# Kernel optimization log

Hardware: AMD Instinct MI355X
Metric: run time of the kernel (lower is better)

## Reference

```python
import jax, jax.numpy as jnp
import numpy as np

M_RANGE = 3
K = 2 * M_RANGE + 1          # kernel size = 7
N_CLASS = K * K              # 49 motion classes
IM_CHANNEL = 3


def setup_inputs() -> dict:
    key = jax.random.key(0)
    k1, k2, k3, k4 = jax.random.split(key, 4)
    B, H, W = 16, 256, 256
    im_input = jax.random.normal(k1, (B, 2 * IM_CHANNEL, H, W), dtype=jnp.float32)
    im_output = jax.random.normal(k2, (B, IM_CHANNEL, H, W), dtype=jnp.float32)
    # motion in [-M_RANGE, M_RANGE-1) so that floor(m)+M_RANGE+1 <= K-1 (valid bin)
    gt_motion = jax.random.uniform(k3, (B, 2, H, W), dtype=jnp.float32) * (2 * M_RANGE - 1) - M_RANGE
    # grouped-conv weight (already in post-swapaxes [n_class, 1, K, K] layout)
    m_kernel = jax.random.uniform(k4, (N_CLASS, 1, K, K), dtype=jnp.float32)
    return {"im_input": im_input, "im_output": im_output,
            "gt_motion": gt_motion, "m_kernel": m_kernel}


def _axis_weights(m):
    # m: [B,H,W] -> bilinear binning weights over K bins: [B,H,W,K]
    f = jnp.floor(m)
    frac = m - f
    idx = f.astype(jnp.int32) + M_RANGE
    oh0 = jax.nn.one_hot(idx, K, dtype=m.dtype)
    oh1 = jax.nn.one_hot(idx + 1, K, dtype=m.dtype)
    return (1.0 - frac)[..., None] * oh0 + frac[..., None] * oh1


def motion2mask(motion):
    # faithful vectorization of the triple-loop: mask[c=iy*K+ix] = b[iy]*a[ix]
    ax = _axis_weights(motion[:, 0])   # x-motion -> columns of ger(b, a)
    ay = _axis_weights(motion[:, 1])   # y-motion -> rows
    mask = ay[..., :, None] * ax[..., None, :]       # [B,H,W,K,K] outer product
    B, H, W = motion.shape[0], motion.shape[2], motion.shape[3]
    return mask.reshape(B, H, W, N_CLASS).transpose(0, 3, 1, 2)  # [B,N_CLASS,H,W]


def _conv(x, w, groups):
    return jax.lax.conv_general_dilated(
        x, w, window_strides=(1, 1),
        padding=[(M_RANGE, M_RANGE), (M_RANGE, M_RANGE)],
        dimension_numbers=("NCHW", "OIHW", "NCHW"),
        feature_group_count=groups)


def reference(im_input, im_output, gt_motion, m_kernel):
    m_mask = motion2mask(gt_motion)                   # [B,N_CLASS,H,W]
    out_mask = _conv(m_mask, m_kernel, N_CLASS)       # grouped conv, same shape
    im = im_input[:, -IM_CHANNEL:]                    # [B,3,H,W]
    B, C, H, W = im.shape
    # construct_image: each channel expanded to N_CLASS copies then grouped-conv
    # == plain conv of each single channel with all N_CLASS kernels
    nearby = _conv(im.reshape(B * C, 1, H, W), m_kernel, 1)
    nearby = nearby.reshape(B, C, N_CLASS, H, W)
    pred = (nearby * out_mask[:, None]).sum(axis=2)   # [B,3,H,W]
    return pred, m_mask
```

## Files before the change

### kernel.cpp

```cpp
#include <hip/hip_runtime.h>
#include <hip/hip_fp16.h>

typedef _Float16 f16x8 __attribute__((ext_vector_type(8)));
typedef float    f32x4 __attribute__((ext_vector_type(4)));

#define TILE   16
#define HALO   22
#define KK     7
#define NCLASS 49
#define IMW    256
#define IMH    256
#define HW     65536
#define HH     484
#define NV     42
#define WHST   52

#define OFF_OMV    0
#define OFF_HALOF  10752
#define OFF_HALOB  11236
#define OFF_KV     11357
#define SH_TOTAL   13415
#define OFF_IML64  10752
#define OFF_IML32  11720

__device__ __forceinline__ unsigned h2u(__half2 h) { union { __half2 h; unsigned u; } c; c.h = h; return c.u; }
__device__ __forceinline__ __half2  u2h(unsigned u) { union { __half2 h; unsigned u; } c; c.u = u; return c.h; }

__global__ __launch_bounds__(256, 3)
void gtnet_kernel(const float* __restrict__ im_input,
                  const float* __restrict__ gt_motion,
                  const float* __restrict__ m_kernel,
                  float* __restrict__ out_pred,
                  float* __restrict__ out_mask)
{
    __shared__ __align__(16) unsigned SH[SH_TOTAL];
    unsigned*      const omV    = SH + OFF_OMV;
    unsigned*      const haloF  = SH + OFF_HALOF;
    unsigned char* const haloB8 = (unsigned char*)(SH + OFF_HALOB);
    unsigned*      const KV     = SH + OFF_KV;
    float2*        const iml64  = (float2*)(SH + OFF_IML64);
    float*         const iml32  = (float*)(SH + OFF_IML32);
    __half*        const Whf    = (__half*)SH;

    const int tid  = threadIdx.x;
    const int lane = tid & 63, wv_id = tid >> 6;
    const int tx = tid & 15, ty = tid >> 4;
    const int x0 = blockIdx.x * TILE, y0 = blockIdx.y * TILE;
    const int b  = blockIdx.z;
    const int x = x0 + tx, y = y0 + ty;

    const float* mot_x = gt_motion + (size_t)b * 2 * HW;
    const float* mot_y = mot_x + HW;
    const float* imP   = im_input + ((size_t)b * 6 + 3) * HW;

    float2 imr01[2]; float imr2[2];
    #pragma unroll
    for (int k = 0; k < 2; k++) {
        int i = tid + k * 256;
        float2 v01 = make_float2(0.0f, 0.0f); float v2 = 0.0f;
        if (i < HH) {
            int hy = i / HALO, hx = i - hy * HALO;
            int gy = y0 - 3 + hy, gx = x0 - 3 + hx;
            if (gy >= 0 && gy < IMH && gx >= 0 && gx < IMW) {
                int off = gy * IMW + gx;
                v01.x = imP[off];
                v01.y = imP[off + HW];
                v2    = imP[off + 2 * HW];
            }
        }
        imr01[k] = v01; imr2[k] = v2;
    }

    for (int i = tid; i < NCLASS * NV; i += 256) {
        int s = i / NV, n = i - s * NV;
        float k0 = m_kernel[n * NCLASS + s];
        float k7 = m_kernel[(n + KK) * NCLASS + s];
        KV[i] = h2u(__halves2half2(__float2half_rn(k0), __float2half_rn(k7)));
    }
    #pragma unroll
    for (int k = 0; k < 2; k++) {
        int i = tid + k * 256;
        if (i < HH) {
            int hy = i / HALO, hx = i - hy * HALO;
            int gy = y0 - 3 + hy, gx = x0 - 3 + hx;
            unsigned pf = 0u, n4b = 255u;
            if (gy >= 0 && gy < IMH && gx >= 0 && gx < IMW) {
                int off = gy * IMW + gx;
                float ay = mot_y[off] + 3.0f;
                float ax = mot_x[off] + 3.0f;
                float iyf = floorf(ay), ixf = floorf(ax);
                float fy = ay - iyf,    fx = ax - ixf;
                int n00 = (int)iyf * KK + (int)ixf;
                n00 = (n00 < 0) ? 0 : ((n00 > 40) ? 40 : n00);
                pf  = h2u(__halves2half2(__float2half_rn(fy), __float2half_rn(fx)));
                n4b = (unsigned)(n00 * 4);
            }
            haloF[i]  = pf;
            haloB8[i] = (unsigned char)n4b;
        }
    }
    {
        uint4* p = reinterpret_cast<uint4*>(omV);
        for (int i = tid; i < (2 * NV * 128) / 4; i += 256) p[i] = make_uint4(0, 0, 0, 0);
    }

    __syncthreads();

    {
        int off = y * IMW + x;
        float ay = mot_y[off] + 3.0f;
        float ax = mot_x[off] + 3.0f;
        float iyf = floorf(ay), ixf = floorf(ax);
        float fy = ay - iyf,    fx = ax - ixf;
        int   iy = (int)iyf,    ix = (int)ixf;
        float wyA[KK], wxB[KK];
        #pragma unroll
        for (int a = 0; a < KK; a++) {
            wyA[a] = (a == iy) ? (1.0f - fy) : ((a == iy + 1) ? fy : 0.0f);
            wxB[a] = (a == ix) ? (1.0f - fx) : ((a == ix + 1) ? fx : 0.0f);
        }
        float* mm = out_mask + (size_t)b * NCLASS * HW + off;
        #pragma unroll
        for (int a = 0; a < KK; a++)
            #pragma unroll
            for (int bb = 0; bb < KK; bb++)
                mm[(size_t)(a * KK + bb) * HW] = wyA[a] * wxB[bb];
    }

    unsigned* const omHalf = omV + (tid >> 7) * (NV * 128) + (tid & 127);
    const __half hone = __float2half_rn(1.0f);
    #pragma unroll
    for (int u = 0; u < KK; u++) {
        #pragma unroll
        for (int v = 0; v < KK; v++) {
            const int s = u * KK + v;
            const int q = (ty + u) * HALO + (tx + v);
            unsigned pf  = haloF[q];
            unsigned n4u = (unsigned)haloB8[q];
            unsigned n4  = (n4u == 255u) ? 0u : n4u;
            __half2 f2 = u2h(pf);
            __half fy = __low2half(f2), fx = __high2half(f2);
            unsigned wyb = h2u(__halves2half2(__hsub(hone, fy), fy));
            wyb = (n4u == 255u) ? 0u : wyb;
            __half2 wy  = u2h(wyb);
            __half2 wxl = __half2half2(__hsub(hone, fx));
            __half2 wxh = __half2half2(fx);
            const unsigned* kp =
                (const unsigned*)((const char*)KV + s * (NV * 4) + n4);
            unsigned kvA = kp[0], kvB = kp[1];
            unsigned* ob = (unsigned*)((char*)omHalf + n4 * 128);
            unsigned o0 = ob[0], o1 = ob[128];
            __half2 cA = __hmul2(__hmul2(wy, wxl), u2h(kvA));
            __half2 cB = __hmul2(__hmul2(wy, wxh), u2h(kvB));
            ob[0]   = h2u(__hadd2(u2h(o0), cA));
            ob[128] = h2u(__hadd2(u2h(o1), cB));
        }
    }

    __syncthreads();

    #pragma unroll
    for (int k = 0; k < 2; k++) {
        int i = tid + k * 256;
        if (i < HH) { iml64[i] = imr01[k]; iml32[i] = imr2[k]; }
    }

    f16x8 bfr[2][4];
    #pragma unroll
    for (int kit = 0; kit < 2; kit++) {
        #pragma unroll
        for (int nt = 0; nt < 4; nt++) {
            int t  = nt * 16 + (lane & 15);
            int tc = (t > 48) ? 48 : t;
            int k0 = kit * 32 + (lane >> 4) * 8;
            union { unsigned u[4]; f16x8 v; } bu;
            #pragma unroll
            for (int j = 0; j < 4; j++) {
                int c0 = k0 + 2 * j;
                float lo = (c0 <= 48) ? m_kernel[c0 * NCLASS + tc]       : 0.0f;
                float hi = (c0 <= 47) ? m_kernel[(c0 + 1) * NCLASS + tc] : 0.0f;
                bu.u[j] = h2u(__halves2half2(__float2half_rn(lo), __float2half_rn(hi)));
            }
            bfr[kit][nt] = bu.v;
        }
    }

    f16x8 af[2][4];
    #pragma unroll
    for (int kit = 0; kit < 2; kit++) {
        #pragma unroll
        for (int mt = 0; mt < 4; mt++) {
            int k0  = kit * 32 + (lane >> 4) * 8;
            int px  = wv_id * 64 + mt * 16 + (lane & 15);
            const unsigned* pxb = omV + (px >> 7) * (NV * 128) + (px & 127);
            union { unsigned u[4]; f16x8 v; } au;
            #pragma unroll
            for (int j = 0; j < 4; j++) {
                int c0 = k0 + 2 * j;
                int rl = (c0 > 40) ? 40 : c0;
                unsigned d0 = pxb[rl * 128], d1 = pxb[rl * 128 + 128];
                unsigned loM = (d0 & 0xffffu) | (d1 << 16);
                loM = (c0 <= 40) ? loM : 0u;
                int r0 = c0 - 7; r0 = (r0 < 0) ? 0 : ((r0 > 41) ? 41 : r0);
                int r1 = c0 - 6; r1 = (r1 < 0) ? 0 : ((r1 > 41) ? 41 : r1);
                unsigned e0 = pxb[r0 * 128];
                unsigned e1 = pxb[r1 * 128];
                e0 = (c0 >= 8 && c0 <= 48) ? e0 : 0u;
                e1 = (c0 >= 6 && c0 <= 48) ? e1 : 0u;
                unsigned hiM = (e0 >> 16) | (e1 & 0xffff0000u);
                au.u[j] = h2u(__hadd2(u2h(loM), u2h(hiM)));
            }
            af[kit][mt] = au.v;
        }
    }

    __syncthreads();

    f32x4 acc[4][4];
    #pragma unroll
    for (int mt = 0; mt < 4; mt++) {
        #pragma unroll
        for (int nt = 0; nt < 4; nt++) {
            f32x4 c = {0.0f, 0.0f, 0.0f, 0.0f};
            c = __builtin_amdgcn_mfma_f32_16x16x32_f16(af[0][mt], bfr[0][nt], c, 0, 0, 0);
            c = __builtin_amdgcn_mfma_f32_16x16x32_f16(af[1][mt], bfr[1][nt], c, 0, 0, 0);
            acc[mt][nt] = c;
        }
    }

    #pragma unroll
    for (int mt = 0; mt < 4; mt++) {
        #pragma unroll
        for (int nt = 0; nt < 4; nt++) {
            int t = nt * 16 + (lane & 15);
            if (t < NCLASS) {
                #pragma unroll
                for (int r = 0; r < 4; r++) {
                    int px = wv_id * 64 + mt * 16 + (lane >> 4) * 4 + r;
                    Whf[px * WHST + t] = __float2half_rn(acc[mt][nt][r]);
                }
            }
        }
    }

    __syncthreads();

    union { uint2 v[13]; __half h[52]; } wr;
    const uint2* wp = (const uint2*)(Whf + tid * WHST);
    #pragma unroll
    for (int c = 0; c < 13; c++) wr.v[c] = wp[c];

    float a0 = 0.0f, a1 = 0.0f, a2 = 0.0f;
    #pragma unroll
    for (int p = 0; p < KK; p++) {
        #pragma unroll
        for (int qq = 0; qq < KK; qq++) {
            float wvv = __half2float(wr.h[p * KK + qq]);
            int   hq  = (ty + p) * HALO + (tx + qq);
            float2 i01 = iml64[hq];
            float  i2  = iml32[hq];
            a0 = fmaf(wvv, i01.x, a0);
            a1 = fmaf(wvv, i01.y, a1);
            a2 = fmaf(wvv, i2,    a2);
        }
    }
    float* pr = out_pred + (size_t)b * 3 * HW + y * IMW + x;
    pr[0]      = a0;
    pr[HW]     = a1;
    pr[2 * HW] = a2;
}

extern "C" void kernel_launch(void* const* d_in, const int* in_sizes, int n_in,
                              void* d_out, int out_size, void* d_ws, size_t ws_size,
                              hipStream_t stream) {
    const float* im_input  = (const float*)d_in[0];
    const float* gt_motion = (const float*)d_in[2];
    const float* m_kernel  = (const float*)d_in[3];

    float* pred = (float*)d_out;
    float* mask = pred + (size_t)16 * 3 * HW;

    dim3 grid(IMW / TILE, IMH / TILE, 16);
    dim3 block(256);
    hipLaunchKernelGGL(gtnet_kernel, grid, block, 0, stream,
                       im_input, gt_motion, m_kernel, pred, mask);
}
```

Baseline: 343.7 us.

## Restructure MFMA K-dimension to use packed mask words directly and pack weight stores

Result: faster. 336.7 us (-2.1%).

```diff
diff --git a/kernel.cpp b/kernel.cpp
--- a/kernel.cpp
+++ b/kernel.cpp
@@ -13,7 +13,7 @@
 #define HW     65536
 #define HH     484
 #define NV     42
-#define WHST   52
+#define WROW   34
 
 #define OFF_OMV    0
 #define OFF_HALOF  10752
@@ -40,7 +40,6 @@
     unsigned*      const KV     = SH + OFF_KV;
     float2*        const iml64  = (float2*)(SH + OFF_IML64);
     float*         const iml32  = (float*)(SH + OFF_IML32);
-    __half*        const Whf    = (__half*)SH;
 
     const int tid  = threadIdx.x;
     const int lane = tid & 63, wv_id = tid >> 6;
@@ -165,97 +164,88 @@
         if (i < HH) { iml64[i] = imr01[k]; iml32[i] = imr2[k]; }
     }
 
-    f16x8 bfr[2][4];
-    #pragma unroll
-    for (int kit = 0; kit < 2; kit++) {
+    f32x4 acc[4][4];
+    #pragma unroll
+    for (int mt = 0; mt < 4; mt++)
+        #pragma unroll
+        for (int nt = 0; nt < 4; nt++)
+            acc[mt][nt] = (f32x4){0.0f, 0.0f, 0.0f, 0.0f};
+
+    const int vb0  = (lane >> 4) * 4;
+    const int tcol = lane & 15;
+    #pragma unroll
+    for (int kit = 0; kit < 3; kit++) {
+        f16x8 afk[4];
+        #pragma unroll
+        for (int mt = 0; mt < 4; mt++) {
+            int px = wv_id * 64 + mt * 16 + tcol;
+            const unsigned* pxb = omV + (px >> 7) * (NV * 128) + (px & 127);
+            int vb = kit * 16 + vb0;
+            union { unsigned u[4]; f16x8 v; } au;
+            #pragma unroll
+            for (int j = 0; j < 4; j++) {
+                unsigned d = pxb[(vb + j) * 128];
+                au.u[j] = (vb + j <= 41) ? d : 0u;
+            }
+            afk[mt] = au.v;
+        }
+        f16x8 bfk[4];
         #pragma unroll
         for (int nt = 0; nt < 4; nt++) {
-            int t  = nt * 16 + (lane & 15);
+            int t  = nt * 16 + tcol;
             int tc = (t > 48) ? 48 : t;
-            int k0 = kit * 32 + (lane >> 4) * 8;
             union { unsigned u[4]; f16x8 v; } bu;
             #pragma unroll
             for (int j = 0; j < 4; j++) {
-                int c0 = k0 + 2 * j;
-                float lo = (c0 <= 48) ? m_kernel[c0 * NCLASS + tc]       : 0.0f;
-                float hi = (c0 <= 47) ? m_kernel[(c0 + 1) * NCLASS + tc] : 0.0f;
+                int v = kit * 16 + vb0 + j;
+                float lo = (v <= 41) ? m_kernel[v * NCLASS + tc]        : 0.0f;
+                float hi = (v <= 41) ? m_kernel[(v + KK) * NCLASS + tc] : 0.0f;
                 bu.u[j] = h2u(__halves2half2(__float2half_rn(lo), __float2half_rn(hi)));
             }
-            bfr[kit][nt] = bu.v;
-        }
-    }
-
-    f16x8 af[2][4];
-    #pragma unroll
-    for (int kit = 0; kit < 2; kit++) {
-        #pragma unroll
-        for (int mt = 0; mt < 4; mt++) {
-            int k0  = kit * 32 + (lane >> 4) * 8;
-            int px  = wv_id * 64 + mt * 16 + (lane & 15);
-            const unsigned* pxb = omV + (px >> 7) * (NV * 128) + (px & 127);
-            union { unsigned u[4]; f16x8 v; } au;
-            #pragma unroll
-            for (int j = 0; j < 4; j++) {
-                int c0 = k0 + 2 * j;
-                int rl = (c0 > 40) ? 40 : c0;
-                unsigned d0 = pxb[rl * 128], d1 = pxb[rl * 128 + 128];
-                unsigned loM = (d0 & 0xffffu) | (d1 << 16);
-                loM = (c0 <= 40) ? loM : 0u;
-                int r0 = c0 - 7; r0 = (r0 < 0) ? 0 : ((r0 > 41) ? 41 : r0);
-                int r1 = c0 - 6; r1 = (r1 < 0) ? 0 : ((r1 > 41) ? 41 : r1);
-                unsigned e0 = pxb[r0 * 128];
-                unsigned e1 = pxb[r1 * 128];
-                e0 = (c0 >= 8 && c0 <= 48) ? e0 : 0u;
-                e1 = (c0 >= 6 && c0 <= 48) ? e1 : 0u;
-                unsigned hiM = (e0 >> 16) | (e1 & 0xffff0000u);
-                au.u[j] = h2u(__hadd2(u2h(loM), u2h(hiM)));
-            }
-            af[kit][mt] = au.v;
-        }
-    }
-
-    __syncthreads();
-
-    f32x4 acc[4][4];
+            bfk[nt] = bu.v;
+        }
+        #pragma unroll
+        for (int mt = 0; mt < 4; mt++)
+            #pragma unroll
+            for (int nt = 0; nt < 4; nt++)
+                acc[mt][nt] = __builtin_amdgcn_mfma_f32_16x16x32_f16(afk[mt], bfk[nt], acc[mt][nt], 0, 0, 0);
+    }
+
+    __syncthreads();
+
     #pragma unroll
     for (int mt = 0; mt < 4; mt++) {
         #pragma unroll
-        for (int nt = 0; nt < 4; nt++) {
-            f32x4 c = {0.0f, 0.0f, 0.0f, 0.0f};
-            c = __builtin_amdgcn_mfma_f32_16x16x32_f16(af[0][mt], bfr[0][nt], c, 0, 0, 0);
-            c = __builtin_amdgcn_mfma_f32_16x16x32_f16(af[1][mt], bfr[1][nt], c, 0, 0, 0);
-            acc[mt][nt] = c;
-        }
-    }
-
-    #pragma unroll
-    for (int mt = 0; mt < 4; mt++) {
-        #pragma unroll
-        for (int nt = 0; nt < 4; nt++) {
-            int t = nt * 16 + (lane & 15);
-            if (t < NCLASS) {
-                #pragma unroll
-                for (int r = 0; r < 4; r++) {
-                    int px = wv_id * 64 + mt * 16 + (lane >> 4) * 4 + r;
-                    Whf[px * WHST + t] = __float2half_rn(acc[mt][nt][r]);
-                }
-            }
-        }
-    }
-
-    __syncthreads();
-
-    union { uint2 v[13]; __half h[52]; } wr;
-    const uint2* wp = (const uint2*)(Whf + tid * WHST);
-    #pragma unroll
-    for (int c = 0; c < 13; c++) wr.v[c] = wp[c];
+        for (int r = 0; r < 4; r++) {
+            int px = wv_id * 64 + mt * 16 + (lane >> 4) * 4 + r;
+            unsigned* wrow = SH + px * WROW + tcol;
+            unsigned v0 = h2u(__halves2half2(__float2half_rn(acc[mt][0][r]),
+                                             __float2half_rn(acc[mt][1][r])));
+            unsigned v1 = h2u(__halves2half2(__float2half_rn(acc[mt][2][r]),
+                                             __float2half_rn(acc[mt][3][r])));
+            wrow[0]  = v0;
+            wrow[16] = v1;
+        }
+    }
+
+    __syncthreads();
+
+    union { uint2 q[16]; unsigned d[32]; } wr;
+    const uint2* wp = (const uint2*)(SH + tid * WROW);
+    #pragma unroll
+    for (int c = 0; c < 16; c++) wr.q[c] = wp[c];
+
+    #define WHALF(t) ( (t) < 16 ? __low2half(u2h(wr.d[(t)])) :           \
+                       (t) < 32 ? __high2half(u2h(wr.d[(t) - 16])) :     \
+                       (t) < 48 ? __low2half(u2h(wr.d[(t) - 16])) :      \
+                                  __high2half(u2h(wr.d[16])) )
 
     float a0 = 0.0f, a1 = 0.0f, a2 = 0.0f;
     #pragma unroll
     for (int p = 0; p < KK; p++) {
         #pragma unroll
         for (int qq = 0; qq < KK; qq++) {
-            float wvv = __half2float(wr.h[p * KK + qq]);
+            float wvv = __half2float(WHALF(p * KK + qq));
             int   hq  = (ty + p) * HALO + (tx + qq);
             float2 i01 = iml64[hq];
             float  i2  = iml32[hq];
@@ -264,6 +254,7 @@
             a2 = fmaf(wvv, i2,    a2);
         }
     }
+    #undef WHALF
     float* pr = out_pred + (size_t)b * 3 * HW + y * IMW + x;
     pr[0]      = a0;
     pr[HW]     = a1;
```
